# Performance work log

Measured on AMD Instinct MI355X. Metric: run time of the kernel, lower is better.

## Reference

```python
import jax, jax.numpy as jnp
import numpy as np

N, E, H, ED, L, T = 4096, 65536, 128, 64, 3, 4
FO = H // T  # per-tower output dim (32)


def setup_inputs() -> dict:
    key = jax.random.key(0)
    ks = jax.random.split(key, 32)
    def g(i, shape, s=0.05):
        return jax.random.normal(ks[i], shape, dtype=jnp.float32) * s
    return {
        "x": g(0, (N, H), 1.0),
        "edge_attr": g(1, (E, ED), 1.0),
        "edge_index": jax.random.randint(ks[2], (2, E), 0, N, dtype=jnp.int32),
        "enc_W": g(3, (L, H, ED)), "enc_b": g(4, (L, H)),
        "pre_W": g(5, (L, T, H, 3 * H)), "pre_b": g(6, (L, T, H)),
        "post_W": g(7, (L, T, FO, 4 * H)), "post_b": g(8, (L, T, FO)),
        "lin_W": g(9, (L, H, H)), "lin_b": g(10, (L, H)),
        "gru_Wih": g(11, (3 * H, H)), "gru_Whh": g(12, (3 * H, H)),
        "gru_bih": g(13, (3 * H,)), "gru_bhh": g(14, (3 * H,)),
        "em1_W": g(15, (2 * H, 2 * H)), "em1_b": g(16, (2 * H,)),
        "em2_W": g(17, (2 * ED, 2 * H)), "em2_b": g(18, (2 * ED,)),
        "eu1_W": g(19, (2 * ED, 3 * ED)), "eu1_b": g(20, (2 * ED,)),
        "eu2_W": g(21, (ED, 2 * ED)), "eu2_b": g(22, (ED,)),
    }


def _lin(x, W, b):
    return x @ W.T + b


def _pna_layer(x, ea, src, dst, eW, eb, pW, pb, qW, qb, lW, lb):
    # PNAConv: towers=4, pre_layers=1, post_layers=1, aggr=[max,std,mean], scaler=identity
    n = x.shape[0]
    e = _lin(ea, eW, eb)                                   # edge encoder [E,H]
    h = jnp.concatenate([x[dst], x[src], e], axis=-1)       # [E,3H] (x_i, x_j, e)
    msg = jnp.einsum('ec,tfc->etf', h, pW) + pb             # per-tower pre-MLP [E,T,H]
    cnt = jax.ops.segment_sum(jnp.ones((msg.shape[0],), msg.dtype), dst, n)
    denom = jnp.maximum(cnt, 1.0)[:, None, None]
    mean = jax.ops.segment_sum(msg, dst, n) / denom
    mean2 = jax.ops.segment_sum(msg * msg, dst, n) / denom
    std = jnp.sqrt(jax.nn.relu(mean2 - mean * mean) + 1e-5)
    mx = jax.ops.segment_max(msg, dst, n)
    mx = jnp.where((cnt > 0)[:, None, None], mx, 0.0)
    agg = jnp.concatenate([mx, std, mean], axis=-1)         # [N,T,3H]
    xt = jnp.broadcast_to(x[:, None, :], (n, T, x.shape[1]))
    cat = jnp.concatenate([xt, agg], axis=-1)               # [N,T,4H]
    y = jnp.einsum('ntc,tfc->ntf', cat, qW) + qb            # per-tower post-MLP [N,T,FO]
    return _lin(y.reshape(n, -1), lW, lb)                   # [N,H]


def _gru(x, h, Wih, Whh, bih, bhh):
    gi = x @ Wih.T + bih
    gh = h @ Whh.T + bhh
    ir, iz, ic = jnp.split(gi, 3, axis=-1)
    hr, hz, hc = jnp.split(gh, 3, axis=-1)
    r = jax.nn.sigmoid(ir + hr)
    z = jax.nn.sigmoid(iz + hz)
    c = jnp.tanh(ic + r * hc)
    return (1.0 - z) * c + z * h


def reference(x, edge_attr, enc_W, enc_b, pre_W, pre_b, post_W, post_b, lin_W, lin_b,
              gru_Wih, gru_Whh, gru_bih, gru_bhh, em1_W, em1_b, em2_W, em2_b,
              eu1_W, eu1_b, eu2_W, eu2_b, edge_index):
    src, dst = edge_index[0], edge_index[1]
    out, hstate, ea = x, x, edge_attr
    for i in range(L):
        m = jax.nn.relu(_pna_layer(out, ea, src, dst, enc_W[i], enc_b[i],
                                   pre_W[i], pre_b[i], post_W[i], post_b[i],
                                   lin_W[i], lin_b[i]))
        hstate = _gru(m, hstate, gru_Wih, gru_Whh, gru_bih, gru_bhh)
        out = hstate
        uv = jnp.concatenate([out[src], out[dst]], axis=-1)
        m_ed = jax.nn.relu(_lin(jax.nn.relu(_lin(uv, em1_W, em1_b)), em2_W, em2_b))
        ea = _lin(jax.nn.relu(_lin(jnp.concatenate([m_ed, ea], axis=-1), eu1_W, eu1_b)), eu2_W, eu2_b)
    return (out, ea, out)
```

## Files before the change

### kernel.cpp

```cpp
#include <hip/hip_runtime.h>
#include <hip/hip_bf16.h>
#include <math.h>

#define NN 4096
#define EE 65536
#define HH 128
#define EDD 64
#define THD 512

typedef __bf16 bf16;
typedef __bf16 bf16x8 __attribute__((ext_vector_type(8)));
typedef __bf16 bf16x4 __attribute__((ext_vector_type(4)));
typedef float  floatx4 __attribute__((ext_vector_type(4)));

__global__ __launch_bounds__(256) void k_det0(const void* __restrict__ eaIn,
                                              const int* __restrict__ eidx,
                                              int* __restrict__ dflag,
                                              int* __restrict__ iflag,
                                              int* __restrict__ counts)
{
    int b = blockIdx.x, t = threadIdx.x;
    if (b == 0) {
        if (t < 64) {
            const bf16* p = (const bf16*)eaIn;
// ... 194 lines not shown
            W = Whh; bias = bhh;
        } else {
            m0 = (b & 63) * 64;
            int y = b >> 6;
            isPd = y < 8;
            n0 = (isPd ? y : y - 8) * 64;
            W = Wnode_l + (isPd ? 0 : (size_t)512 * 128);
            bias = bcombx_l;
        }
        const int wm = (wave & 1) * 32, wn = (wave >> 1) * 32;
        const int lrow = tid >> 2, lcol = (tid & 3) * 8;
        floatx4 acc00 = {0,0,0,0}, acc01 = {0,0,0,0}, acc10 = {0,0,0,0}, acc11 = {0,0,0,0};
        for (int k0 = 0; k0 < 128; k0 += 32) {
            bf16x8 av = *(const bf16x8*)(out_bf + (size_t)(m0 + lrow) * 128 + k0 + lcol);
            bf16x8 wv = *(const bf16x8*)(W + (size_t)(n0 + lrow) * 128 + k0 + lcol);
            __syncthreads();
            *(bf16x8*)&As[lrow][lcol] = av;
            *(bf16x8*)&Ws[lrow][lcol] = wv;
            __syncthreads();
            bf16x8 a0 = *(const bf16x8*)&As[wm + fr][fk];
            bf16x8 a1 = *(const bf16x8*)&As[wm + 16 + fr][fk];
            bf16x8 b0 = *(const bf16x8*)&Ws[wn + fr][fk];
            bf16x8 b1 = *(const bf16x8*)&Ws[wn + 16 + fr][fk];
            acc00 = __builtin_amdgcn_mfma_f32_16x16x32_bf16(a0, b0, acc00, 0, 0, 0);
            acc01 = __builtin_amdgcn_mfma_f32_16x16x32_bf16(a0, b1, acc01, 0, 0, 0);
            acc10 = __builtin_amdgcn_mfma_f32_16x16x32_bf16(a1, b0, acc10, 0, 0, 0);
            acc11 = __builtin_amdgcn_mfma_f32_16x16x32_bf16(a1, b1, acc11, 0, 0, 0);
        }
        float vb0 = (isGh || isPd) ? bias[n0 + wn + cc] : 0.f;
        float vb1 = (isGh || isPd) ? bias[n0 + wn + 16 + cc] : 0.f;
        floatx4 accs[2][2] = {{acc00, acc01}, {acc10, acc11}};
#pragma unroll
        for (int mt = 0; mt < 2; mt++)
#pragma unroll
            for (int nt = 0; nt < 2; nt++) {
                float vb = nt ? vb1 : vb0;
#pragma unroll
                for (int i = 0; i < 4; i++) {
                    int gm = m0 + wm + mt * 16 + cr + i;
                    int gn = n0 + wn + nt * 16 + cc;
                    float v = accs[mt][nt][i] + vb;
                    if (isGh)      gh[(size_t)gm * 384 + gn] = v;
                    else if (isPd) Pd[(size_t)gm * 512 + gn] = v;
                    else           Ps[(size_t)gm * 512 + gn] = (bf16)v;
                }
            }
    } else {
        bf16 (*As)[72] = (bf16 (*)[72])smem;
        bf16 (*Ws)[72] = (bf16 (*)[72])(smem + 9216);
        int q = b - 1024;
        const int e0 = (q & 1023) * 64, n0g = (q >> 10) * 256;
#pragma unroll
        for (int v = 0; v < 2; v++) {
            int lin = v * 2048 + tid * 8;
            int r = lin >> 6, c = lin & 63;
            *(bf16x8*)&As[r][c] = *(const bf16x8*)(eaord + (size_t)(e0 + r) * 64 + c);
        }
#pragma unroll
        for (int v = 0; v < 8; v++) {
            int lin = v * 2048 + tid * 8;
            int r = lin >> 6, c = lin & 63;
            *(bf16x8*)&Ws[r][c] = *(const bf16x8*)(wcomb_l + (size_t)(n0g + r) * 64 + c);
        }
        __syncthreads();

        floatx4 acc[4][4];
#pragma unroll
        for (int mt = 0; mt < 4; mt++)
#pragma unroll
            for (int nt = 0; nt < 4; nt++) acc[mt][nt] = (floatx4){0,0,0,0};

#pragma unroll
        for (int kk = 0; kk < 64; kk += 32) {
            bf16x8 af[4], bv[4];
#pragma unroll
            for (int mt = 0; mt < 4; mt++) af[mt] = *(const bf16x8*)&As[mt * 16 + fr][kk + fk];
#pragma unroll
            for (int nt = 0; nt < 4; nt++) bv[nt] = *(const bf16x8*)&Ws[wave * 64 + nt * 16 + fr][kk + fk];
#pragma unroll
            for (int mt = 0; mt < 4; mt++)
#pragma unroll
                for (int nt = 0; nt < 4; nt++)
                    acc[mt][nt] = __builtin_amdgcn_mfma_f32_16x16x32_bf16(af[mt], bv[nt], acc[mt][nt], 0, 0, 0);
        }
#pragma unroll
        for (int mt = 0; mt < 4; mt++)
#pragma unroll
            for (int nt = 0; nt < 4; nt++)
#pragma unroll
                for (int i = 0; i < 4; i++) {
                    int row = mt * 16 + cr + i;
                    int col = n0g + wave * 64 + nt * 16 + cc;
                    Qord[(size_t)(e0 + row) * 512 + col] = (bf16)acc[mt][nt][i];
                }
    }
}

__global__ __launch_bounds__(256) void k_gi(
    const bf16* __restrict__ m_bf, const bf16* __restrict__ Wih,
    const float* __restrict__ bih, float* __restrict__ gi)
{
    __shared__ bf16 As[64][40];
    __shared__ bf16 Ws[64][40];
    const int m0 = blockIdx.x * 64, n0 = blockIdx.y * 64;
    const int tid = threadIdx.x, wave = tid >> 6, lane = tid & 63;
    const int wm = (wave & 1) * 32, wn = (wave >> 1) * 32;
    const int lrow = tid >> 2, lcol = (tid & 3) * 8;
    const int fr = lane & 15, fk = (lane >> 4) * 8;
    floatx4 acc00 = {0,0,0,0}, acc01 = {0,0,0,0}, acc10 = {0,0,0,0}, acc11 = {0,0,0,0};

    for (int k0 = 0; k0 < 128; k0 += 32) {
        bf16x8 av = *(const bf16x8*)(m_bf + (size_t)(m0 + lrow) * 128 + k0 + lcol);
        bf16x8 wv = *(const bf16x8*)(Wih + (size_t)(n0 + lrow) * 128 + k0 + lcol);
        __syncthreads();
        *(bf16x8*)&As[lrow][lcol] = av;
        *(bf16x8*)&Ws[lrow][lcol] = wv;
        __syncthreads();
        bf16x8 a0 = *(const bf16x8*)&As[wm + fr][fk];
        bf16x8 a1 = *(const bf16x8*)&As[wm + 16 + fr][fk];
        bf16x8 b0 = *(const bf16x8*)&Ws[wn + fr][fk];
        bf16x8 b1 = *(const bf16x8*)&Ws[wn + 16 + fr][fk];
        acc00 = __builtin_amdgcn_mfma_f32_16x16x32_bf16(a0, b0, acc00, 0, 0, 0);
        acc01 = __builtin_amdgcn_mfma_f32_16x16x32_bf16(a0, b1, acc01, 0, 0, 0);
        acc10 = __builtin_amdgcn_mfma_f32_16x16x32_bf16(a1, b0, acc10, 0, 0, 0);
        acc11 = __builtin_amdgcn_mfma_f32_16x16x32_bf16(a1, b1, acc11, 0, 0, 0);
    }
    const int cc = lane & 15, cr = (lane >> 4) * 4;
    float vb0 = bih[n0 + wn + cc];
    float vb1 = bih[n0 + wn + 16 + cc];
    floatx4 accs[2][2] = {{acc00, acc01}, {acc10, acc11}};
#pragma unroll
    for (int mt = 0; mt < 2; mt++)
#pragma unroll
        for (int nt = 0; nt < 2; nt++) {
            float vb = nt ? vb1 : vb0;
#pragma unroll
            for (int i = 0; i < 4; i++) {
                int gm = m0 + wm + mt * 16 + cr + i;
                int gn = n0 + wn + nt * 16 + cc;
                gi[(size_t)gm * 384 + gn] = accs[mt][nt][i] + vb;
            }
        }
}

__global__ __launch_bounds__(256) void k_edge(
    const bf16* __restrict__ SAB,
    const bf16* __restrict__ em2W, const float* __restrict__ em2b,
    const bf16* __restrict__ eu1W, const float* __restrict__ eu1b,
    const bf16* __restrict__ eu2W, const float* __restrict__ eu2b,
    const int* __restrict__ src, const int* __restrict__ dst,
    const int* __restrict__ pos,
    bf16* __restrict__ eaord, float* __restrict__ ea_out_f)
{
    __shared__ char smem[53248];
    bf16 (*Ws)[40]   = (bf16 (*)[40])smem;
    bf16 (*med)[200] = (bf16 (*)[200])(smem + 10240);
    bf16 (*As)[40]   = (bf16 (*)[40])(smem + 35840);
    bf16 (*t2s)[136] = (bf16 (*)[136])(smem + 35840);

    const int e0 = blockIdx.x * 64;
    const int tid = threadIdx.x, wave = tid >> 6, lane = tid & 63;
    const int lrow = tid >> 2, lcol = (tid & 3) * 8;
    const int fr = lane & 15, fk = (lane >> 4) * 8;
    const int cc = lane & 15, cr = (lane >> 4) * 4;
    const int wr = tid & 127, wc = (tid >> 7) * 16;
    const int wr3 = tid & 63, wc3 = (tid >> 6) * 8;
    const int sI = src[e0 + lrow], dI = dst[e0 + lrow];
    const floatx4 z4 = {0.f, 0.f, 0.f, 0.f};

    const int ac0 = (tid & 3) * 16;
    const int apr = pos[e0 + lrow];
    bf16x8 ea0 = *(const bf16x8*)(eaord + (size_t)apr * 64 + ac0);
    bf16x8 ea1 = *(const bf16x8*)(eaord + (size_t)apr * 64 + ac0 + 8);

    const int wm1 = (wave & 1) * 32, wn1 = (wave >> 1) * 64;
    floatx4 acc1[2][4];
#pragma unroll
    for (int mt = 0; mt < 2; mt++)
#pragma unroll
        for (int nt = 0; nt < 4; nt++) acc1[mt][nt] = z4;

    bf16x8 sv = *(const bf16x8*)(SAB + (size_t)sI * 512 + lcol);
    bf16x8 dv = *(const bf16x8*)(SAB + (size_t)dI * 512 + 256 + lcol);
    bf16x8 w0 = *(const bf16x8*)(em2W + (size_t)wr * 256 + wc);
    bf16x8 w1 = *(const bf16x8*)(em2W + (size_t)wr * 256 + wc + 8);

    for (int k0 = 0; k0 < 256; k0 += 32) {
        __syncthreads();
        bf16 a8[8];
#pragma unroll
        for (int j = 0; j < 8; j++)
            a8[j] = (bf16)fmaxf((float)sv[j] + (float)dv[j], 0.f);
        *(bf16x8*)&As[lrow][lcol] = *(bf16x8*)a8;
        *(bf16x8*)&Ws[wr][wc]     = w0;
        *(bf16x8*)&Ws[wr][wc + 8] = w1;
        int kn = k0 + 32;
        if (kn < 256) {
            sv = *(const bf16x8*)(SAB + (size_t)sI * 512 + kn + lcol);
            dv = *(const bf16x8*)(SAB + (size_t)dI * 512 + 256 + kn + lcol);
            w0 = *(const bf16x8*)(em2W + (size_t)wr * 256 + kn + wc);
            w1 = *(const bf16x8*)(em2W + (size_t)wr * 256 + kn + wc + 8);
        } else {
            w0 = *(const bf16x8*)(eu1W + (size_t)wr * 192 + wc);
            w1 = *(const bf16x8*)(eu1W + (size_t)wr * 192 + wc + 8);
        }
        __syncthreads();
        bf16x8 af[2], bv[4];
        af[0] = *(const bf16x8*)&As[wm1 + fr][fk];
        af[1] = *(const bf16x8*)&As[wm1 + 16 + fr][fk];
#pragma unroll
        for (int nt = 0; nt < 4; nt++) bv[nt] = *(const bf16x8*)&Ws[wn1 + nt * 16 + fr][fk];
#pragma unroll
        for (int mt = 0; mt < 2; mt++)
#pragma unroll
            for (int nt = 0; nt < 4; nt++)
                acc1[mt][nt] = __builtin_amdgcn_mfma_f32_16x16x32_bf16(af[mt], bv[nt], acc1[mt][nt], 0, 0, 0);
    }
#pragma unroll
    for (int mt = 0; mt < 2; mt++)
#pragma unroll
        for (int nt = 0; nt < 4; nt++)
#pragma unroll
            for (int i = 0; i < 4; i++) {
                int row = wm1 + mt * 16 + cr + i;
                int col = wn1 + nt * 16 + cc;
                med[row][col] = (bf16)fmaxf(acc1[mt][nt][i] + em2b[col], 0.f);
            }
    *(bf16x8*)&med[lrow][128 + ac0]     = ea0;
    *(bf16x8*)&med[lrow][128 + ac0 + 8] = ea1;

    floatx4 acc2[2][4];
#pragma unroll
    for (int mt = 0; mt < 2; mt++)
#pragma unroll
        for (int nt = 0; nt < 4; nt++) acc2[mt][nt] = z4;

    for (int k0 = 0; k0 < 192; k0 += 32) {
        __syncthreads();
        *(bf16x8*)&Ws[wr][wc]     = w0;
        *(bf16x8*)&Ws[wr][wc + 8] = w1;
        int kn = k0 + 32;
        if (kn < 192) {
            w0 = *(const bf16x8*)(eu1W + (size_t)wr * 192 + kn + wc);
            w1 = *(const bf16x8*)(eu1W + (size_t)wr * 192 + kn + wc + 8);
        } else {
            w0 = *(const bf16x8*)(eu2W + (size_t)wr3 * 128 + wc3);
        }
        __syncthreads();
        bf16x8 af[2], bv[4];
        af[0] = *(const bf16x8*)&med[wm1 + fr][k0 + fk];
        af[1] = *(const bf16x8*)&med[wm1 + 16 + fr][k0 + fk];
#pragma unroll
        for (int nt = 0; nt < 4; nt++) bv[nt] = *(const bf16x8*)&Ws[wn1 + nt * 16 + fr][fk];
#pragma unroll
        for (int mt = 0; mt < 2; mt++)
#pragma unroll
            for (int nt = 0; nt < 4; nt++)
                acc2[mt][nt] = __builtin_amdgcn_mfma_f32_16x16x32_bf16(af[mt], bv[nt], acc2[mt][nt], 0, 0, 0);
    }
#pragma unroll
    for (int mt = 0; mt < 2; mt++)
#pragma unroll
        for (int nt = 0; nt < 4; nt++)
#pragma unroll
            for (int i = 0; i < 4; i++) {
                int row = wm1 + mt * 16 + cr + i;
                int col = wn1 + nt * 16 + cc;
                t2s[row][col] = (bf16)fmaxf(acc2[mt][nt][i] + eu1b[col], 0.f);
            }

    const int wm3 = (wave & 1) * 32, wn3 = (wave >> 1) * 32;
    floatx4 acc3[2][2];
#pragma unroll
    for (int mt = 0; mt < 2; mt++)
#pragma unroll
        for (int nt = 0; nt < 2; nt++) acc3[mt][nt] = z4;

    for (int k0 = 0; k0 < 128; k0 += 32) {
        __syncthreads();
        *(bf16x8*)&Ws[wr3][wc3] = w0;
        int kn = k0 + 32;
        if (kn < 128)
            w0 = *(const bf16x8*)(eu2W + (size_t)wr3 * 128 + kn + wc3);
        __syncthreads();
        bf16x8 af[2], bv[2];
        af[0] = *(const bf16x8*)&t2s[wm3 + fr][k0 + fk];
        af[1] = *(const bf16x8*)&t2s[wm3 + 16 + fr][k0 + fk];
#pragma unroll
        for (int nt = 0; nt < 2; nt++) bv[nt] = *(const bf16x8*)&Ws[wn3 + nt * 16 + fr][fk];
#pragma unroll
        for (int mt = 0; mt < 2; mt++)
#pragma unroll
            for (int nt = 0; nt < 2; nt++)
                acc3[mt][nt] = __builtin_amdgcn_mfma_f32_16x16x32_bf16(af[mt], bv[nt], acc3[mt][nt], 0, 0, 0);
    }
#pragma unroll
    for (int mt = 0; mt < 2; mt++)
#pragma unroll
        for (int nt = 0; nt < 2; nt++)
#pragma unroll
            for (int i = 0; i < 4; i++) {
                int row = wm3 + mt * 16 + cr + i;
                int col = wn3 + nt * 16 + cc;
                float v = acc3[mt][nt][i] + eu2b[col];
                int e = e0 + row;
                eaord[(size_t)pos[e] * 64 + col] = (bf16)v;
                if (ea_out_f) ea_out_f[(size_t)e * 64 + col] = v;
            }
}

__global__ __launch_bounds__(256) void k_postg(
    const bf16* __restrict__ xin, const bf16* __restrict__ aggX,
    const bf16* __restrict__ aggS, const bf16* __restrict__ aggM,
    const bf16* __restrict__ qWbf, const float* __restrict__ qb,
    bf16* __restrict__ ybf)
{
    __shared__ bf16 As[64][40];
    __shared__ bf16 Ws[32][40];
    const int n0 = blockIdx.x * 64, t = blockIdx.y;
    const int tid = threadIdx.x, wave = tid >> 6, lane = tid & 63;
    const int lrow = tid >> 2, lcol = (tid & 3) * 8;
    const int fr = lane & 15, fk = (lane >> 4) * 8;
    floatx4 acc0 = {0,0,0,0}, acc1 = {0,0,0,0};

    for (int k0 = 0; k0 < 512; k0 += 32) {
        int n = n0 + lrow;
        int c0 = k0 + lcol;
        const bf16* srcp;
        if (c0 < 128)      srcp = xin  + (size_t)n * 128 + c0;
        else if (c0 < 256) srcp = aggX + (size_t)n * 512 + t * 128 + (c0 - 128);
        else if (c0 < 384) srcp = aggS + (size_t)n * 512 + t * 128 + (c0 - 256);
        else               srcp = aggM + (size_t)n * 512 + t * 128 + (c0 - 384);
        bf16x8 a8 = *(const bf16x8*)srcp;
        bf16 w8[8];
        if (tid < 128) {
            int wr = tid >> 2, wc = (tid & 3) * 8;
            *(bf16x8*)w8 = *(const bf16x8*)(qWbf + (size_t)(t * 32 + wr) * 512 + k0 + wc);
        }
        __syncthreads();
        *(bf16x8*)&As[lrow][lcol] = a8;
        if (tid < 128) {
            int wr = tid >> 2, wc = (tid & 3) * 8;
            *(bf16x8*)&Ws[wr][wc] = *(bf16x8*)w8;
        }
        __syncthreads();
        bf16x8 a  = *(const bf16x8*)&As[wave * 16 + fr][fk];
        bf16x8 b0 = *(const bf16x8*)&Ws[fr][fk];
        bf16x8 b1 = *(const bf16x8*)&Ws[16 + fr][fk];
        acc0 = __builtin_amdgcn_mfma_f32_16x16x32_bf16(a, b0, acc0, 0, 0, 0);
        acc1 = __builtin_amdgcn_mfma_f32_16x16x32_bf16(a, b1, acc1, 0, 0, 0);
    }
    const int cc = lane & 15, cr = (lane >> 4) * 4;
#pragma unroll
    for (int i = 0; i < 4; i++) {
        int gn = n0 + wave * 16 + cr + i;
        ybf[(size_t)gn * 128 + t * 32 + cc]      = (bf16)(acc0[i] + qb[t * 32 + cc]);
        ybf[(size_t)gn * 128 + t * 32 + 16 + cc] = (bf16)(acc1[i] + qb[t * 32 + 16 + cc]);
    }
}

__global__ __launch_bounds__(1024) void k_scan(
    const int* __restrict__ counts, int* __restrict__ offs, int* __restrict__ cursor)
{
    __shared__ int ls[1024];
    int tid = threadIdx.x, base = tid * 4;
    int c0 = counts[base], c1 = counts[base + 1], c2 = counts[base + 2], c3 = counts[base + 3];
    ls[tid] = c0 + c1 + c2 + c3;
    __syncthreads();
    for (int d = 1; d < 1024; d <<= 1) {
        int v = (tid >= d) ? ls[tid - d] : 0;
        __syncthreads();
        ls[tid] += v;
        __syncthreads();
    }
    int r = tid ? ls[tid - 1] : 0;
    offs[base] = r;     cursor[base] = r;     r += c0;
    offs[base + 1] = r; cursor[base + 1] = r; r += c1;
    offs[base + 2] = r; cursor[base + 2] = r; r += c2;
    offs[base + 3] = r; cursor[base + 3] = r; r += c3;
    if (tid == 1023) offs[4096] = r;
}

__global__ void k_fill(const int* __restrict__ dst, const int* __restrict__ srcW,
                       int* __restrict__ cursor, int* __restrict__ pos,
                       int* __restrict__ srcord)
{
    int e = blockIdx.x * 256 + threadIdx.x;
    int p = atomicAdd(&cursor[dst[e]], 1);
    pos[e] = p;
    srcord[p] = srcW[e];
}

__global__ __launch_bounds__(128) void k_agg(
    const float* __restrict__ Pd, const bf16* __restrict__ Ps,
    const bf16* __restrict__ Qord,
    const int* __restrict__ srcord, const int* __restrict__ offs,
    bf16* __restrict__ aggX, bf16* __restrict__ aggS, bf16* __restrict__ aggM)
{
    int n = blockIdx.x, tid = threadIdx.x;
    int c = tid * 4;
    float4 pd = *(const float4*)(Pd + (size_t)n * 512 + c);
    float s0 = 0, s1 = 0, s2 = 0, s3 = 0;
    float q0 = 0, q1 = 0, q2 = 0, q3 = 0;
    float x0 = -3e38f, x1 = -3e38f, x2 = -3e38f, x3 = -3e38f;
    int beg = offs[n], end = offs[n + 1];
    for (int i = beg; i < end; i++) {
        int sn = srcord[i];
        bf16x4 psv = *(const bf16x4*)(Ps + (size_t)sn * 512 + c);
        bf16x4 qv  = *(const bf16x4*)(Qord + (size_t)i * 512 + c);
        float m0 = pd.x + (float)psv[0] + (float)qv[0];
        float m1 = pd.y + (float)psv[1] + (float)qv[1];
        float m2 = pd.z + (float)psv[2] + (float)qv[2];
        float m3 = pd.w + (float)psv[3] + (float)qv[3];
        s0 += m0; s1 += m1; s2 += m2; s3 += m3;
        q0 += m0 * m0; q1 += m1 * m1; q2 += m2 * m2; q3 += m3 * m3;
        x0 = fmaxf(x0, m0); x1 = fmaxf(x1, m1); x2 = fmaxf(x2, m2); x3 = fmaxf(x3, m3);
    }
    int cnt = end - beg;
    float inv = 1.f / fmaxf((float)cnt, 1.f);
    float me0 = s0 * inv, me1 = s1 * inv, me2 = s2 * inv, me3 = s3 * inv;
    float v0 = fmaxf(q0 * inv - me0 * me0, 0.f);
    float v1 = fmaxf(q1 * inv - me1 * me1, 0.f);
    float v2 = fmaxf(q2 * inv - me2 * me2, 0.f);
    float v3 = fmaxf(q3 * inv - me3 * me3, 0.f);
    size_t o = (size_t)n * 512 + c;
    bf16x4 mx, st, me;
    mx[0] = (bf16)(cnt > 0 ? x0 : 0.f); mx[1] = (bf16)(cnt > 0 ? x1 : 0.f);
    mx[2] = (bf16)(cnt > 0 ? x2 : 0.f); mx[3] = (bf16)(cnt > 0 ? x3 : 0.f);
    st[0] = (bf16)sqrtf(v0 + 1e-5f); st[1] = (bf16)sqrtf(v1 + 1e-5f);
    st[2] = (bf16)sqrtf(v2 + 1e-5f); st[3] = (bf16)sqrtf(v3 + 1e-5f);
    me[0] = (bf16)me0; me[1] = (bf16)me1; me[2] = (bf16)me2; me[3] = (bf16)me3;
    *(bf16x4*)(aggX + o) = mx;
    *(bf16x4*)(aggS + o) = st;
    *(bf16x4*)(aggM + o) = me;
}

__global__ void k_gru(const float* __restrict__ gi, const float* __restrict__ gh,
                      float* __restrict__ hst, bf16* __restrict__ ob,
                      float* __restrict__ fo)
{
    int i = blockIdx.x * 256 + threadIdx.x;
    int k = i & 127;
    size_t b = (size_t)(i >> 7) * 384;
    float ir = gi[b + k],       hr = gh[b + k];
    float iz = gi[b + 128 + k], hz = gh[b + 128 + k];
    float ic = gi[b + 256 + k], hc = gh[b + 256 + k];
    float r = 1.f / (1.f + __expf(-(ir + hr)));
    float z = 1.f / (1.f + __expf(-(iz + hz)));
    float c = tanhf(ic + r * hc);
    float h = hst[i];
    float hn = (1.f - z) * c + z * h;
    hst[i] = hn;
    ob[i] = (bf16)hn;
    if (fo) { fo[i] = hn; fo[4718592 + i] = hn; }
}

__global__ void k_sentinel(float* __restrict__ o, float v)
{
    int i = blockIdx.x * 256 + threadIdx.x;
    o[i] = v;
}

extern "C" void kernel_launch(void* const* d_in, const int* in_sizes, int n_in,
                              void* d_out, int out_size, void* d_ws, size_t ws_size,
                              hipStream_t stream)
{
    static const int exp_sizes[23] = {
        524288, 4194304, 131072, 24576, 384, 589824, 1536, 196608, 384,
        49152, 384, 49152, 49152, 384, 384, 65536, 256, 32768, 128,
        24576, 128, 8192, 64 };
    if (n_in != 23) { k_sentinel<<<2048, 256, 0, stream>>>((float*)d_out, 200.f); return; }
    for (int i = 0; i < 23; i++)
        if (in_sizes[i] != exp_sizes[i]) {
            k_sentinel<<<2048, 256, 0, stream>>>((float*)d_out, 60.f + 4.f * i);
            return;
        }
    if (out_size != 5242880) { k_sentinel<<<2048, 256, 0, stream>>>((float*)d_out, 52.f); return; }

    const int* eidx = (const int*)d_in[2];

    char* w = (char*)d_ws;
    size_t off = 0;
    auto alloc = [&](size_t bytes) -> char* {
        char* p = w + off;
        off = (off + bytes + 255) & ~(size_t)255;
        return p;
    };
    int*   dflag   = (int*)  alloc(256);
    int*   iflag   = (int*)  alloc(256);
    int*   srcW    = (int*)  alloc((size_t)EE * 4);
    int*   dstW    = (int*)  alloc((size_t)EE * 4);
    int*   pos     = (int*)  alloc((size_t)EE * 4);
    int*   srcord  = (int*)  alloc((size_t)EE * 4);
    float* out_f32 = (float*)alloc((size_t)NN * HH * 4);
    bf16*  out_bf  = (bf16*) alloc((size_t)NN * HH * 2);
    bf16*  m_bf    = (bf16*) alloc((size_t)NN * HH * 2);
    bf16*  ybf     = (bf16*) alloc((size_t)NN * HH * 2);
    bf16*  eaord   = (bf16*) alloc((size_t)EE * EDD * 2);
    bf16*  wcombAll= (bf16*) alloc((size_t)3 * THD * EDD * 2);
    float* bcombAll= (float*)alloc((size_t)3 * 1024 * 4);
    int*   counts  = (int*)  alloc((size_t)NN * 4);
    int*   offs    = (int*)  alloc((size_t)(NN + 1) * 4);
    int*   cursor  = (int*)  alloc((size_t)NN * 4);
    float* Pd      = (float*)alloc((size_t)NN * THD * 4);
    bf16*  Ps      = (bf16*) alloc((size_t)NN * THD * 2);
    bf16*  aggX    = (bf16*) alloc((size_t)NN * THD * 2);
    bf16*  aggS    = (bf16*) alloc((size_t)NN * THD * 2);
    bf16*  aggM    = (bf16*) alloc((size_t)NN * THD * 2);
    float* giB     = (float*)alloc((size_t)NN * 384 * 4);
    float* ghB     = (float*)alloc((size_t)NN * 384 * 4);
    float* encWc  = (float*)alloc((size_t)24576 * 4);
    float* encbc  = (float*)alloc((size_t)384 * 4);
    float* preWc  = (float*)alloc((size_t)589824 * 4);
    float* prebc  = (float*)alloc((size_t)1536 * 4);
    float* postbc = (float*)alloc((size_t)384 * 4);
    float* linbc  = (float*)alloc((size_t)384 * 4);
    float* bihc   = (float*)alloc((size_t)384 * 4);
    float* bhhc   = (float*)alloc((size_t)384 * 4);
    float* em1bc  = (float*)alloc((size_t)256 * 4);
    float* em1ext = (float*)alloc((size_t)512 * 4);
    float* em2bc  = (float*)alloc((size_t)128 * 4);
    float* eu1bc  = (float*)alloc((size_t)128 * 4);
    float* eu2bc  = (float*)alloc((size_t)64 * 4);
    bf16* preWbf = (bf16*)alloc((size_t)589824 * 2);
    bf16* WnodeBf= (bf16*)alloc((size_t)3 * 131072 * 2);
    bf16* postWbf= (bf16*)alloc((size_t)196608 * 2);
    bf16* linWbf = (bf16*)alloc((size_t)49152 * 2);
    bf16* WihBf  = (bf16*)alloc((size_t)49152 * 2);
    bf16* WhhBf  = (bf16*)alloc((size_t)49152 * 2);
    bf16* em1Wbf = (bf16*)alloc((size_t)65536 * 2);
    bf16* Wem1Bf = (bf16*)alloc((size_t)65536 * 2);
    bf16* em2Wbf = (bf16*)alloc((size_t)32768 * 2);
    bf16* eu1Wbf = (bf16*)alloc((size_t)24576 * 2);
    bf16* eu2Wbf = (bf16*)alloc((size_t)8192 * 2);
    char* region = alloc((size_t)EE * 512 * 2);
    bf16*  Qord = (bf16*) (region);
    bf16*  SAB  = (bf16*) (region);

    if (ws_size < off) { k_sentinel<<<2048, 256, 0, stream>>>((float*)d_out, 44.f); return; }

    k_det0<<<18, 256, 0, stream>>>(d_in[1], eidx, dflag, iflag, counts);
    k_extcnt<<<EE / 256, 256, 0, stream>>>(eidx, srcW, dstW, iflag, counts);
    k_scan<<<1, 1024, 0, stream>>>(counts, offs, cursor);
    k_fill<<<EE / 256, 256, 0, stream>>>(dstW, srcW, cursor, pos, srcord);

    {
        JobTab tab;
        int bi = 0, ji = 0;
        auto add = [&](const void* s, void* d1, void* d2, int n, int mode) {
            tab.j[ji] = { s, d1, d2, n, mode, bi };
            bi += (n + 255) / 256;
            ji++;
        };
        add(d_in[0],  out_f32, out_bf, 524288, 2);
        add(d_in[1],  eaord,   nullptr, 4194304, 3);
        add(d_in[5],  preWc,   preWbf, 589824, 2);
        add(d_in[3],  encWc,   nullptr, 24576, 0);
        add(d_in[4],  encbc,   nullptr, 384, 0);
        add(d_in[6],  prebc,   nullptr, 1536, 0);
        add(d_in[8],  postbc,  nullptr, 384, 0);
        add(d_in[10], linbc,   nullptr, 384, 0);
        add(d_in[13], bihc,    nullptr, 384, 0);
        add(d_in[14], bhhc,    nullptr, 384, 0);
        add(d_in[16], em1bc,   nullptr, 256, 0);
        add(d_in[18], em2bc,   nullptr, 128, 0);
        add(d_in[20], eu1bc,   nullptr, 128, 0);
        add(d_in[22], eu2bc,   nullptr, 64, 0);
        add(d_in[7],  postWbf, nullptr, 196608, 1);
        add(d_in[9],  linWbf,  nullptr, 49152, 1);
        add(d_in[11], WihBf,   nullptr, 49152, 1);
        add(d_in[12], WhhBf,   nullptr, 49152, 1);
        add(d_in[15], em1Wbf,  nullptr, 65536, 1);
        add(d_in[17], em2Wbf,  nullptr, 32768, 1);
        add(d_in[19], eu1Wbf,  nullptr, 24576, 1);
        add(d_in[21], eu2Wbf,  nullptr, 8192, 1);
        k_canon_all<<<bi, 256, 0, stream>>>(tab, dflag, pos);
    }
    k_setup2<<<2178, 256, 0, stream>>>(preWbf, em1Wbf, em1bc, WnodeBf, Wem1Bf, em1ext,
                                       preWc, encWc, encbc, prebc, wcombAll, bcombAll);

    auto GEMM = [&](const bf16* A, int lda, const bf16* Wm, int ldw, const float* bias,
                    void* C, int ldc, int M, int Nout, int K, bool relu, int om) {
        dim3 grid(M / 64, Nout / 64);
        if (relu) {
            if (om) k_mgemm<true, 1><<<grid, 256, 0, stream>>>(A, lda, Wm, ldw, bias, C, ldc, K);
            else    k_mgemm<true, 0><<<grid, 256, 0, stream>>>(A, lda, Wm, ldw, bias, C, ldc, K);
        } else {
            if (om) k_mgemm<false, 1><<<grid, 256, 0, stream>>>(A, lda, Wm, ldw, bias, C, ldc, K);
            else    k_mgemm<false, 0><<<grid, 256, 0, stream>>>(A, lda, Wm, ldw, bias, C, ldc, K);
        }
    };

    for (int l = 0; l < 3; l++) {
        const bf16*  Wnode_l  = WnodeBf + (size_t)l * 131072;
        const bf16*  postW_l  = postWbf + (size_t)l * 65536;
        const float* postb_l  = postbc + (size_t)l * 128;
        const bf16*  linW_l   = linWbf + (size_t)l * 16384;
        const float* linb_l   = linbc  + (size_t)l * 128;
        const bf16*  wcomb_l  = wcombAll + (size_t)l * 32768;
        const float* bcombx_l = bcombAll + (size_t)l * 1024;
        const bool last = (l == 2);

        k_pna_front<<<3456, 256, 0, stream>>>(out_bf, Wnode_l, bcombx_l, Pd, Ps,
                                              eaord, wcomb_l, Qord, WhhBf, bhhc, ghB);
        k_agg<<<NN, 128, 0, stream>>>(Pd, Ps, Qord, srcord, offs, aggX, aggS, aggM);
        k_postg<<<dim3(NN / 64, 4), 256, 0, stream>>>(out_bf, aggX, aggS, aggM,
                                                      postW_l, postb_l, ybf);
        GEMM(ybf, HH, linW_l, HH, linb_l, m_bf, HH, NN, HH, HH, true, 1);
        k_gi<<<dim3(64, 6), 256, 0, stream>>>(m_bf, WihBf, bihc, giB);
        k_gru<<<NN * HH / 256, 256, 0, stream>>>(giB, ghB, out_f32, out_bf,
                                                 last ? (float*)d_out : (float*)nullptr);
        GEMM(out_bf, HH, Wem1Bf, 128, em1ext, SAB, 512, NN, 512, HH, false, 1);
        k_edge<<<EE / 64, 256, 0, stream>>>(SAB, em2Wbf, em2bc, eu1Wbf, eu1bc,
                                            eu2Wbf, eu2bc, srcW, dstW, pos,
                                            eaord, last ? (float*)d_out + 524288 : (float*)nullptr);
    }
}
```

Baseline: 445.2 us.

## Load edge MLP MFMA operands directly from global into registers, drop LDS staging

The edge-update kernel no longer stages the gathered node features and weight tiles through shared memory with two barriers per k-step. Each lane now loads its MFMA A and B fragments straight from global memory in fragment layout, double-buffered in registers. Only the intermediate activations still go through LDS, with one barrier between stages. This removes per-iteration barriers and LDS traffic and lowers the shared-memory footprint. In exchange, global loads are less coalesced and weight rows are fetched redundantly by the two waves that share the same columns.

```diff
diff --git a/kernel.cpp b/kernel.cpp
--- a/kernel.cpp
+++ b/kernel.cpp
@@ -370,69 +370,75 @@
     const int* __restrict__ pos,
     bf16* __restrict__ eaord, float* __restrict__ ea_out_f)
 {
-    __shared__ char smem[53248];
-    bf16 (*Ws)[40]   = (bf16 (*)[40])smem;
-    bf16 (*med)[200] = (bf16 (*)[200])(smem + 10240);
-    bf16 (*As)[40]   = (bf16 (*)[40])(smem + 35840);
-    bf16 (*t2s)[136] = (bf16 (*)[136])(smem + 35840);
+    __shared__ char smem[43008];
+    bf16 (*med)[200] = (bf16 (*)[200])smem;
+    bf16 (*t2s)[136] = (bf16 (*)[136])(smem + 25600);
 
     const int e0 = blockIdx.x * 64;
     const int tid = threadIdx.x, wave = tid >> 6, lane = tid & 63;
-    const int lrow = tid >> 2, lcol = (tid & 3) * 8;
     const int fr = lane & 15, fk = (lane >> 4) * 8;
     const int cc = lane & 15, cr = (lane >> 4) * 4;
-    const int wr = tid & 127, wc = (tid >> 7) * 16;
-    const int wr3 = tid & 63, wc3 = (tid >> 6) * 8;
-    const int sI = src[e0 + lrow], dI = dst[e0 + lrow];
     const floatx4 z4 = {0.f, 0.f, 0.f, 0.f};
-
-    const int ac0 = (tid & 3) * 16;
-    const int apr = pos[e0 + lrow];
+    const int wm1 = (wave & 1) * 32, wn1 = (wave >> 1) * 64;
+    const int wm3 = (wave & 1) * 32, wn3 = (wave >> 1) * 32;
+
+    const int ar = tid >> 2, ac0 = (tid & 3) * 16;
+    const int apr = pos[e0 + ar];
     bf16x8 ea0 = *(const bf16x8*)(eaord + (size_t)apr * 64 + ac0);
     bf16x8 ea1 = *(const bf16x8*)(eaord + (size_t)apr * 64 + ac0 + 8);
 
-    const int wm1 = (wave & 1) * 32, wn1 = (wave >> 1) * 64;
+    const int r0 = wm1 + fr, r1 = wm1 + 16 + fr;
+    const int s0I = src[e0 + r0], d0I = dst[e0 + r0];
+    const int s1I = src[e0 + r1], d1I = dst[e0 + r1];
+
     floatx4 acc1[2][4];
 #pragma unroll
     for (int mt = 0; mt < 2; mt++)
 #pragma unroll
         for (int nt = 0; nt < 4; nt++) acc1[mt][nt] = z4;
 
-    bf16x8 sv = *(const bf16x8*)(SAB + (size_t)sI * 512 + lcol);
-    bf16x8 dv = *(const bf16x8*)(SAB + (size_t)dI * 512 + 256 + lcol);
-    bf16x8 w0 = *(const bf16x8*)(em2W + (size_t)wr * 256 + wc);
-    bf16x8 w1 = *(const bf16x8*)(em2W + (size_t)wr * 256 + wc + 8);
+    bf16x8 as0 = *(const bf16x8*)(SAB + (size_t)s0I * 512 + fk);
+    bf16x8 ad0 = *(const bf16x8*)(SAB + (size_t)d0I * 512 + 256 + fk);
+    bf16x8 as1 = *(const bf16x8*)(SAB + (size_t)s1I * 512 + fk);
+    bf16x8 ad1 = *(const bf16x8*)(SAB + (size_t)d1I * 512 + 256 + fk);
+    bf16x8 bw0 = *(const bf16x8*)(em2W + (size_t)(wn1 +      fr) * 256 + fk);
+    bf16x8 bw1 = *(const bf16x8*)(em2W + (size_t)(wn1 + 16 + fr) * 256 + fk);
+    bf16x8 bw2 = *(const bf16x8*)(em2W + (size_t)(wn1 + 32 + fr) * 256 + fk);
+    bf16x8 bw3 = *(const bf16x8*)(em2W + (size_t)(wn1 + 48 + fr) * 256 + fk);
 
     for (int k0 = 0; k0 < 256; k0 += 32) {
-        __syncthreads();
-        bf16 a8[8];
-#pragma unroll
-        for (int j = 0; j < 8; j++)
-            a8[j] = (bf16)fmaxf((float)sv[j] + (float)dv[j], 0.f);
-        *(bf16x8*)&As[lrow][lcol] = *(bf16x8*)a8;
-        *(bf16x8*)&Ws[wr][wc]     = w0;
-        *(bf16x8*)&Ws[wr][wc + 8] = w1;
+        bf16 a0[8], a1[8];
+#pragma unroll
+        for (int j = 0; j < 8; j++) {
+            a0[j] = (bf16)fmaxf((float)as0[j] + (float)ad0[j], 0.f);
+            a1[j] = (bf16)fmaxf((float)as1[j] + (float)ad1[j], 0.f);
+        }
+        bf16x8 b0 = bw0, b1 = bw1, b2 = bw2, b3 = bw3;
         int kn = k0 + 32;
         if (kn < 256) {
-            sv = *(const bf16x8*)(SAB + (size_t)sI * 512 + kn + lcol);
-            dv = *(const bf16x8*)(SAB + (size_t)dI * 512 + 256 + kn + lcol);
-            w0 = *(const bf16x8*)(em2W + (size_t)wr * 256 + kn + wc);
-            w1 = *(const bf16x8*)(em2W + (size_t)wr * 256 + kn + wc + 8);
+            as0 = *(const bf16x8*)(SAB + (size_t)s0I * 512 + kn + fk);
+            ad0 = *(const bf16x8*)(SAB + (size_t)d0I * 512 + 256 + kn + fk);
+            as1 = *(const bf16x8*)(SAB + (size_t)s1I * 512 + kn + fk);
+            ad1 = *(const bf16x8*)(SAB + (size_t)d1I * 512 + 256 + kn + fk);
+            bw0 = *(const bf16x8*)(em2W + (size_t)(wn1 +      fr) * 256 + kn + fk);
+            bw1 = *(const bf16x8*)(em2W + (size_t)(wn1 + 16 + fr) * 256 + kn + fk);
+            bw2 = *(const bf16x8*)(em2W + (size_t)(wn1 + 32 + fr) * 256 + kn + fk);
+            bw3 = *(const bf16x8*)(em2W + (size_t)(wn1 + 48 + fr) * 256 + kn + fk);
         } else {
-            w0 = *(const bf16x8*)(eu1W + (size_t)wr * 192 + wc);
-            w1 = *(const bf16x8*)(eu1W + (size_t)wr * 192 + wc + 8);
-        }
-        __syncthreads();
-        bf16x8 af[2], bv[4];
-        af[0] = *(const bf16x8*)&As[wm1 + fr][fk];
-        af[1] = *(const bf16x8*)&As[wm1 + 16 + fr][fk];
-#pragma unroll
-        for (int nt = 0; nt < 4; nt++) bv[nt] = *(const bf16x8*)&Ws[wn1 + nt * 16 + fr][fk];
-#pragma unroll
-        for (int mt = 0; mt < 2; mt++)
-#pragma unroll
-            for (int nt = 0; nt < 4; nt++)
-                acc1[mt][nt] = __builtin_amdgcn_mfma_f32_16x16x32_bf16(af[mt], bv[nt], acc1[mt][nt], 0, 0, 0);
+            bw0 = *(const bf16x8*)(eu1W + (size_t)(wn1 +      fr) * 192 + fk);
+            bw1 = *(const bf16x8*)(eu1W + (size_t)(wn1 + 16 + fr) * 192 + fk);
+            bw2 = *(const bf16x8*)(eu1W + (size_t)(wn1 + 32 + fr) * 192 + fk);
+            bw3 = *(const bf16x8*)(eu1W + (size_t)(wn1 + 48 + fr) * 192 + fk);
+        }
+        bf16x8 av0 = *(bf16x8*)a0, av1 = *(bf16x8*)a1;
+        acc1[0][0] = __builtin_amdgcn_mfma_f32_16x16x32_bf16(av0, b0, acc1[0][0], 0, 0, 0);
+        acc1[0][1] = __builtin_amdgcn_mfma_f32_16x16x32_bf16(av0, b1, acc1[0][1], 0, 0, 0);
+        acc1[0][2] = __builtin_amdgcn_mfma_f32_16x16x32_bf16(av0, b2, acc1[0][2], 0, 0, 0);
+        acc1[0][3] = __builtin_amdgcn_mfma_f32_16x16x32_bf16(av0, b3, acc1[0][3], 0, 0, 0);
+        acc1[1][0] = __builtin_amdgcn_mfma_f32_16x16x32_bf16(av1, b0, acc1[1][0], 0, 0, 0);
+        acc1[1][1] = __builtin_amdgcn_mfma_f32_16x16x32_bf16(av1, b1, acc1[1][1], 0, 0, 0);
+        acc1[1][2] = __builtin_amdgcn_mfma_f32_16x16x32_bf16(av1, b2, acc1[1][2], 0, 0, 0);
+        acc1[1][3] = __builtin_amdgcn_mfma_f32_16x16x32_bf16(av1, b3, acc1[1][3], 0, 0, 0);
     }
 #pragma unroll
     for (int mt = 0; mt < 2; mt++)
@@ -444,8 +450,9 @@
                 int col = wn1 + nt * 16 + cc;
                 med[row][col] = (bf16)fmaxf(acc1[mt][nt][i] + em2b[col], 0.f);
             }
-    *(bf16x8*)&med[lrow][128 + ac0]     = ea0;
-    *(bf16x8*)&med[lrow][128 + ac0 + 8] = ea1;
+    *(bf16x8*)&med[ar][128 + ac0]     = ea0;
+    *(bf16x8*)&med[ar][128 + ac0 + 8] = ea1;
+    __syncthreads();
 
     floatx4 acc2[2][4];
 #pragma unroll
@@ -454,27 +461,27 @@
         for (int nt = 0; nt < 4; nt++) acc2[mt][nt] = z4;
 
     for (int k0 = 0; k0 < 192; k0 += 32) {
-        __syncthreads();
-        *(bf16x8*)&Ws[wr][wc]     = w0;
-        *(bf16x8*)&Ws[wr][wc + 8] = w1;
+        bf16x8 af0 = *(const bf16x8*)&med[wm1 +      fr][k0 + fk];
+        bf16x8 af1 = *(const bf16x8*)&med[wm1 + 16 + fr][k0 + fk];
+        bf16x8 b0 = bw0, b1 = bw1, b2 = bw2, b3 = bw3;
         int kn = k0 + 32;
         if (kn < 192) {
-            w0 = *(const bf16x8*)(eu1W + (size_t)wr * 192 + kn + wc);
-            w1 = *(const bf16x8*)(eu1W + (size_t)wr * 192 + kn + wc + 8);
+            bw0 = *(const bf16x8*)(eu1W + (size_t)(wn1 +      fr) * 192 + kn + fk);
+            bw1 = *(const bf16x8*)(eu1W + (size_t)(wn1 + 16 + fr) * 192 + kn + fk);
+            bw2 = *(const bf16x8*)(eu1W + (size_t)(wn1 + 32 + fr) * 192 + kn + fk);
+            bw3 = *(const bf16x8*)(eu1W + (size_t)(wn1 + 48 + fr) * 192 + kn + fk);
         } else {
-            w0 = *(const bf16x8*)(eu2W + (size_t)wr3 * 128 + wc3);
-        }
-        __syncthreads();
-        bf16x8 af[2], bv[4];
-        af[0] = *(const bf16x8*)&med[wm1 + fr][k0 + fk];
-        af[1] = *(const bf16x8*)&med[wm1 + 16 + fr][k0 + fk];
-#pragma unroll
-        for (int nt = 0; nt < 4; nt++) bv[nt] = *(const bf16x8*)&Ws[wn1 + nt * 16 + fr][fk];
-#pragma unroll
-        for (int mt = 0; mt < 2; mt++)
-#pragma unroll
-            for (int nt = 0; nt < 4; nt++)
-                acc2[mt][nt] = __builtin_amdgcn_mfma_f32_16x16x32_bf16(af[mt], bv[nt], acc2[mt][nt], 0, 0, 0);
+            bw0 = *(const bf16x8*)(eu2W + (size_t)(wn3 +      fr) * 128 + fk);
+            bw1 = *(const bf16x8*)(eu2W + (size_t)(wn3 + 16 + fr) * 128 + fk);
+        }
+        acc2[0][0] = __builtin_amdgcn_mfma_f32_16x16x32_bf16(af0, b0, acc2[0][0], 0, 0, 0);
+        acc2[0][1] = __builtin_amdgcn_mfma_f32_16x16x32_bf16(af0, b1, acc2[0][1], 0, 0, 0);
+        acc2[0][2] = __builtin_amdgcn_mfma_f32_16x16x32_bf16(af0, b2, acc2[0][2], 0, 0, 0);
+        acc2[0][3] = __builtin_amdgcn_mfma_f32_16x16x32_bf16(af0, b3, acc2[0][3], 0, 0, 0);
+        acc2[1][0] = __builtin_amdgcn_mfma_f32_16x16x32_bf16(af1, b0, acc2[1][0], 0, 0, 0);
+        acc2[1][1] = __builtin_amdgcn_mfma_f32_16x16x32_bf16(af1, b1, acc2[1][1], 0, 0, 0);
+        acc2[1][2] = __builtin_amdgcn_mfma_f32_16x16x32_bf16(af1, b2, acc2[1][2], 0, 0, 0);
+        acc2[1][3] = __builtin_amdgcn_mfma_f32_16x16x32_bf16(af1, b3, acc2[1][3], 0, 0, 0);
     }
 #pragma unroll
     for (int mt = 0; mt < 2; mt++)
@@ -486,8 +493,8 @@
                 int col = wn1 + nt * 16 + cc;
                 t2s[row][col] = (bf16)fmaxf(acc2[mt][nt][i] + eu1b[col], 0.f);
             }
-
-    const int wm3 = (wave & 1) * 32, wn3 = (wave >> 1) * 32;
+    __syncthreads();
+
     floatx4 acc3[2][2];
 #pragma unroll
     for (int mt = 0; mt < 2; mt++)
@@ -495,22 +502,18 @@
         for (int nt = 0; nt < 2; nt++) acc3[mt][nt] = z4;
 
     for (int k0 = 0; k0 < 128; k0 += 32) {
-        __syncthreads();
-        *(bf16x8*)&Ws[wr3][wc3] = w0;
+        bf16x8 af0 = *(const bf16x8*)&t2s[wm3 +      fr][k0 + fk];
+        bf16x8 af1 = *(const bf16x8*)&t2s[wm3 + 16 + fr][k0 + fk];
+        bf16x8 b0 = bw0, b1 = bw1;
         int kn = k0 + 32;
-        if (kn < 128)
-            w0 = *(const bf16x8*)(eu2W + (size_t)wr3 * 128 + kn + wc3);
-        __syncthreads();
-        bf16x8 af[2], bv[2];
-        af[0] = *(const bf16x8*)&t2s[wm3 + fr][k0 + fk];
-        af[1] = *(const bf16x8*)&t2s[wm3 + 16 + fr][k0 + fk];
-#pragma unroll
-        for (int nt = 0; nt < 2; nt++) bv[nt] = *(const bf16x8*)&Ws[wn3 + nt * 16 + fr][fk];
-#pragma unroll
-        for (int mt = 0; mt < 2; mt++)
-#pragma unroll
-            for (int nt = 0; nt < 2; nt++)
-                acc3[mt][nt] = __builtin_amdgcn_mfma_f32_16x16x32_bf16(af[mt], bv[nt], acc3[mt][nt], 0, 0, 0);
+        if (kn < 128) {
+            bw0 = *(const bf16x8*)(eu2W + (size_t)(wn3 +      fr) * 128 + kn + fk);
+            bw1 = *(const bf16x8*)(eu2W + (size_t)(wn3 + 16 + fr) * 128 + kn + fk);
+        }
+        acc3[0][0] = __builtin_amdgcn_mfma_f32_16x16x32_bf16(af0, b0, acc3[0][0], 0, 0, 0);
+        acc3[0][1] = __builtin_amdgcn_mfma_f32_16x16x32_bf16(af0, b1, acc3[0][1], 0, 0, 0);
+        acc3[1][0] = __builtin_amdgcn_mfma_f32_16x16x32_bf16(af1, b0, acc3[1][0], 0, 0, 0);
+        acc3[1][1] = __builtin_amdgcn_mfma_f32_16x16x32_bf16(af1, b1, acc3[1][1], 0, 0, 0);
     }
 #pragma unroll
     for (int mt = 0; mt < 2; mt++)
```

Result: slower. 518.7 us (+16.5%).

## Fuse per-tower post-MLP and linear layer into one kernel via LDS

Applied to the files above, without the earlier changes.

Merges the per-tower post GEMM and the following linear+ReLU GEMM into a single kernel. Each block computes all four towers for 64 nodes, keeps the 64x128 intermediate in shared memory, and then applies the linear layer directly. This removes one launch and the global write and read of the intermediate buffer. In exchange, the grid drops from 256 blocks to 64 on a chip with many CUs, and each block now serially loops over the towers, so parallelism falls sharply.

```diff
diff --git a/kernel.cpp b/kernel.cpp
--- a/kernel.cpp
+++ b/kernel.cpp
@@ -527,53 +527,91 @@
             }
 }
 
-__global__ __launch_bounds__(256) void k_postg(
+__global__ __launch_bounds__(256) void k_postlin(
     const bf16* __restrict__ xin, const bf16* __restrict__ aggX,
     const bf16* __restrict__ aggS, const bf16* __restrict__ aggM,
     const bf16* __restrict__ qWbf, const float* __restrict__ qb,
-    bf16* __restrict__ ybf)
+    const bf16* __restrict__ linW, const float* __restrict__ linb,
+    bf16* __restrict__ m_out)
 {
     __shared__ bf16 As[64][40];
-    __shared__ bf16 Ws[32][40];
-    const int n0 = blockIdx.x * 64, t = blockIdx.y;
+    __shared__ bf16 Wb[64][40];
+    __shared__ bf16 ylds[64][136];
+    const int n0 = blockIdx.x * 64;
     const int tid = threadIdx.x, wave = tid >> 6, lane = tid & 63;
     const int lrow = tid >> 2, lcol = (tid & 3) * 8;
     const int fr = lane & 15, fk = (lane >> 4) * 8;
-    floatx4 acc0 = {0,0,0,0}, acc1 = {0,0,0,0};
-
-    for (int k0 = 0; k0 < 512; k0 += 32) {
-        int n = n0 + lrow;
-        int c0 = k0 + lcol;
-        const bf16* srcp;
-        if (c0 < 128)      srcp = xin  + (size_t)n * 128 + c0;
-        else if (c0 < 256) srcp = aggX + (size_t)n * 512 + t * 128 + (c0 - 128);
-        else if (c0 < 384) srcp = aggS + (size_t)n * 512 + t * 128 + (c0 - 256);
-        else               srcp = aggM + (size_t)n * 512 + t * 128 + (c0 - 384);
-        bf16x8 a8 = *(const bf16x8*)srcp;
-        bf16 w8[8];
-        if (tid < 128) {
-            int wr = tid >> 2, wc = (tid & 3) * 8;
-            *(bf16x8*)w8 = *(const bf16x8*)(qWbf + (size_t)(t * 32 + wr) * 512 + k0 + wc);
-        }
-        __syncthreads();
-        *(bf16x8*)&As[lrow][lcol] = a8;
-        if (tid < 128) {
-            int wr = tid >> 2, wc = (tid & 3) * 8;
-            *(bf16x8*)&Ws[wr][wc] = *(bf16x8*)w8;
-        }
-        __syncthreads();
-        bf16x8 a  = *(const bf16x8*)&As[wave * 16 + fr][fk];
-        bf16x8 b0 = *(const bf16x8*)&Ws[fr][fk];
-        bf16x8 b1 = *(const bf16x8*)&Ws[16 + fr][fk];
-        acc0 = __builtin_amdgcn_mfma_f32_16x16x32_bf16(a, b0, acc0, 0, 0, 0);
-        acc1 = __builtin_amdgcn_mfma_f32_16x16x32_bf16(a, b1, acc1, 0, 0, 0);
-    }
     const int cc = lane & 15, cr = (lane >> 4) * 4;
-#pragma unroll
-    for (int i = 0; i < 4; i++) {
-        int gn = n0 + wave * 16 + cr + i;
-        ybf[(size_t)gn * 128 + t * 32 + cc]      = (bf16)(acc0[i] + qb[t * 32 + cc]);
-        ybf[(size_t)gn * 128 + t * 32 + 16 + cc] = (bf16)(acc1[i] + qb[t * 32 + 16 + cc]);
+
+    for (int t = 0; t < 4; t++) {
+        floatx4 acc0 = {0,0,0,0}, acc1 = {0,0,0,0};
+        for (int k0 = 0; k0 < 512; k0 += 32) {
+            int n = n0 + lrow;
+            int c0 = k0 + lcol;
+            const bf16* srcp;
+            if (c0 < 128)      srcp = xin  + (size_t)n * 128 + c0;
+            else if (c0 < 256) srcp = aggX + (size_t)n * 512 + t * 128 + (c0 - 128);
+            else if (c0 < 384) srcp = aggS + (size_t)n * 512 + t * 128 + (c0 - 256);
+            else               srcp = aggM + (size_t)n * 512 + t * 128 + (c0 - 384);
+            bf16x8 a8 = *(const bf16x8*)srcp;
+            bf16 w8[8];
+            if (tid < 128) {
+                int wrr = tid >> 2, wcc = (tid & 3) * 8;
+                *(bf16x8*)w8 = *(const bf16x8*)(qWbf + (size_t)(t * 32 + wrr) * 512 + k0 + wcc);
+            }
+            __syncthreads();
+            *(bf16x8*)&As[lrow][lcol] = a8;
+            if (tid < 128) {
+                int wrr = tid >> 2, wcc = (tid & 3) * 8;
+                *(bf16x8*)&Wb[wrr][wcc] = *(bf16x8*)w8;
+            }
+            __syncthreads();
+            bf16x8 a  = *(const bf16x8*)&As[wave * 16 + fr][fk];
+            bf16x8 b0 = *(const bf16x8*)&Wb[fr][fk];
+            bf16x8 b1 = *(const bf16x8*)&Wb[16 + fr][fk];
+            acc0 = __builtin_amdgcn_mfma_f32_16x16x32_bf16(a, b0, acc0, 0, 0, 0);
+            acc1 = __builtin_amdgcn_mfma_f32_16x16x32_bf16(a, b1, acc1, 0, 0, 0);
+        }
+#pragma unroll
+        for (int i = 0; i < 4; i++) {
+            int row = wave * 16 + cr + i;
+            ylds[row][t * 32 + cc]      = (bf16)(acc0[i] + qb[t * 32 + cc]);
+            ylds[row][t * 32 + 16 + cc] = (bf16)(acc1[i] + qb[t * 32 + 16 + cc]);
+        }
+    }
+
+    const int wm = (wave & 1) * 32, wn = (wave >> 1) * 32;
+    for (int nh = 0; nh < 128; nh += 64) {
+        floatx4 acc00 = {0,0,0,0}, acc01 = {0,0,0,0}, acc10 = {0,0,0,0}, acc11 = {0,0,0,0};
+        for (int k0 = 0; k0 < 128; k0 += 32) {
+            bf16x8 wv = *(const bf16x8*)(linW + (size_t)(nh + lrow) * 128 + k0 + lcol);
+            __syncthreads();
+            *(bf16x8*)&Wb[lrow][lcol] = wv;
+            __syncthreads();
+            bf16x8 a0 = *(const bf16x8*)&ylds[wm + fr][k0 + fk];
+            bf16x8 a1 = *(const bf16x8*)&ylds[wm + 16 + fr][k0 + fk];
+            bf16x8 b0 = *(const bf16x8*)&Wb[wn + fr][fk];
+            bf16x8 b1 = *(const bf16x8*)&Wb[wn + 16 + fr][fk];
+            acc00 = __builtin_amdgcn_mfma_f32_16x16x32_bf16(a0, b0, acc00, 0, 0, 0);
+            acc01 = __builtin_amdgcn_mfma_f32_16x16x32_bf16(a0, b1, acc01, 0, 0, 0);
+            acc10 = __builtin_amdgcn_mfma_f32_16x16x32_bf16(a1, b0, acc10, 0, 0, 0);
+            acc11 = __builtin_amdgcn_mfma_f32_16x16x32_bf16(a1, b1, acc11, 0, 0, 0);
+        }
+        float vb0 = linb[nh + wn + cc];
+        float vb1 = linb[nh + wn + 16 + cc];
+        floatx4 accs[2][2] = {{acc00, acc01}, {acc10, acc11}};
+#pragma unroll
+        for (int mt = 0; mt < 2; mt++)
+#pragma unroll
+            for (int nt = 0; nt < 2; nt++) {
+                float vb = nt ? vb1 : vb0;
+#pragma unroll
+                for (int i = 0; i < 4; i++) {
+                    int gm = n0 + wm + mt * 16 + cr + i;
+                    int gn = nh + wn + nt * 16 + cc;
+                    m_out[(size_t)gm * 128 + gn] = (bf16)fmaxf(accs[mt][nt][i] + vb, 0.f);
+                }
+            }
     }
 }
 
@@ -713,7 +751,6 @@
     float* out_f32 = (float*)alloc((size_t)NN * HH * 4);
     bf16*  out_bf  = (bf16*) alloc((size_t)NN * HH * 2);
     bf16*  m_bf    = (bf16*) alloc((size_t)NN * HH * 2);
-    bf16*  ybf     = (bf16*) alloc((size_t)NN * HH * 2);
     bf16*  eaord   = (bf16*) alloc((size_t)EE * EDD * 2);
     bf16*  wcombAll= (bf16*) alloc((size_t)3 * THD * EDD * 2);
     float* bcombAll= (float*)alloc((size_t)3 * 1024 * 4);
@@ -822,9 +859,8 @@
         k_pna_front<<<3456, 256, 0, stream>>>(out_bf, Wnode_l, bcombx_l, Pd, Ps,
                                               eaord, wcomb_l, Qord, WhhBf, bhhc, ghB);
         k_agg<<<NN, 128, 0, stream>>>(Pd, Ps, Qord, srcord, offs, aggX, aggS, aggM);
-        k_postg<<<dim3(NN / 64, 4), 256, 0, stream>>>(out_bf, aggX, aggS, aggM,
-                                                      postW_l, postb_l, ybf);
-        GEMM(ybf, HH, linW_l, HH, linb_l, m_bf, HH, NN, HH, HH, true, 1);
+        k_postlin<<<64, 256, 0, stream>>>(out_bf, aggX, aggS, aggM,
+                                          postW_l, postb_l, linW_l, linb_l, m_bf);
         k_gi<<<dim3(64, 6), 256, 0, stream>>>(m_bf, WihBf, bihc, giB);
         k_gru<<<NN * HH / 256, 256, 0, stream>>>(giB, ghB, out_f32, out_bf,
                                                  last ? (float*)d_out : (float*)nullptr);
```

Result: slower. 492.0 us (+10.5%).
